# Kernel tuning notes

Hardware: AMD Instinct MI355X
Metric: run time of the kernel (lower is better)

The kernel has to match this reference:

```python
import jax, jax.numpy as jnp
import numpy as np
import math
from jax import lax

B, L, D, P, V, K = 4, 2048, 512, 128, 8, 4


def _lin(x, w, b):
    # torch Linear: y = x @ W^T + b, W shape (out, in)
    return jnp.einsum('...i,oi->...o', x, w) + b


def _gelu(v):
    return jax.nn.gelu(v, approximate=False)


def _dwconv_causal(x_ncl, w, b):
    # depthwise causal conv: torch Conv1d(groups=D, padding=K-1) then [:, :, :L]
    y = lax.conv_general_dilated(x_ncl, w, (1,), [(K - 1, 0)],
                                 dimension_numbers=('NCH', 'OIH', 'NCH'),
                                 feature_group_count=D)
    return y + b[None, :, None]


def _ln(v, g, b):
    m = v.mean(-1, keepdims=True)
    var = v.var(-1, keepdims=True)
    return (v - m) / jnp.sqrt(var + 1e-5) * g + b


def setup_inputs() -> dict:
    key = jax.random.key(0)
    it = iter(jax.random.split(key, 64))
    def nrm(shape, s=0.02):
        return jax.random.normal(next(it), shape, dtype=jnp.float32) * s
    z = lambda *s: jnp.zeros(s, jnp.float32)
    return dict(
        x=nrm((B, L, D), 1.0),
        lc_w=nrm((D, 1, K)), lc_b=z(D),
        cg_w=nrm((D, 1, K)), cg_b=z(D),
        cp_w=nrm((D, D)), cp_b=z(D),
        tw_w=nrm((D, D)), tw_b=z(D),
        omega_scale=jnp.full((D,), 0.01, jnp.float32),
        pi0_w=nrm((D, D)), pi0_b=z(D),
        pi2_w=nrm((D, D)), pi2_b=z(D),
        m1v_w=nrm((D, D)), m1v_b=z(D),
        m1o_w=nrm((D, D)), m1o_b=z(D),
        mag_w=nrm((D, D)), mag_b=z(D),
        mag_scale=jnp.asarray(5.0, jnp.float32),
        qo_w=nrm((D, D)), qo_b=z(D),
        ke_w=nrm((P, D)), ke_b=z(P),
        ve_w=nrm((V, D)), ve_b=z(V),
        sk0_w=nrm((D, 2 * D)), sk0_b=z(D),
        sk2_w=nrm((P, D)), sk2_b=z(P),
        sg_w=nrm((1, D)), sg_b=z(1),
        kvo_w=nrm((D, V)), kvo_b=z(D),
        ln_g=jnp.ones(5 * D, jnp.float32), ln_b=z(5 * D),
        o1_w=nrm((2 * D, 5 * D)), o1_b=z(2 * D),
        o2_w=nrm((D, 2 * D)), o2_b=z(D),
    )


def reference(x, lc_w, lc_b, cg_w, cg_b, cp_w, cp_b, tw_w, tw_b, omega_scale,
              pi0_w, pi0_b, pi2_w, pi2_b, m1v_w, m1v_b, m1o_w, m1o_b,
              mag_w, mag_b, mag_scale, qo_w, qo_b, ke_w, ke_b, ve_w, ve_b,
              sk0_w, sk0_b, sk2_w, sk2_b, sg_w, sg_b, kvo_w, kvo_b,
              ln_g, ln_b, o1_w, o1_b, o2_w, o2_b):
    Bs, Ls, Ds = x.shape
    # local gated causal depthwise conv branch
    xc = jnp.transpose(x, (0, 2, 1))                          # (B, D, L)
    co = _dwconv_causal(xc, lc_w, lc_b)
    cg = jax.nn.sigmoid(_dwconv_causal(xc, cg_w, cg_b))
    conv_out = _lin(jnp.transpose(co * cg, (0, 2, 1)), cp_w, cp_b)
    # evolving phases
    omega_scaled = _lin(x, tw_w, tw_b) * jnp.abs(omega_scale)
    phi = _lin(_gelu(_lin(x, pi0_w, pi0_b)), pi2_w, pi2_b) + jnp.cumsum(omega_scaled, axis=1)
    cos_phi = jnp.cos(phi)
    sin_phi = jnp.sin(phi)
    # magnitude-weighted phase memory
    v1 = _lin(x, m1v_w, m1v_b)
    magnitude = jax.nn.sigmoid(_lin(x, mag_w, mag_b)) * jnp.abs(mag_scale)
    wv1 = magnitude * v1
    sqrt_mag = jnp.sqrt(jnp.cumsum(magnitude, axis=1) + 1e-8)
    mem1_cos = jnp.cumsum(wv1 * cos_phi, axis=1) / sqrt_mag
    mem1_sin = jnp.cumsum(wv1 * sin_phi, axis=1) / sqrt_mag
    phi_q = phi + _lin(x, qo_w, qo_b)
    pos_ret = (mem1_cos * jnp.cos(phi_q) + mem1_sin * jnp.sin(phi_q)) / math.sqrt(Ds)
    pos_out = _lin(pos_ret, m1o_w, m1o_b)
    # phase-keyed associative KV memory
    query_phase = jnp.tanh(_lin(x, ke_w, ke_b)) * math.pi    # (B, L, P)
    values = _lin(x, ve_w, ve_b)                              # (B, L, V)
    store_gate = jax.nn.sigmoid(_lin(x, sg_w, sg_b))          # (B, L, 1)
    positions = jnp.arange(1, Ls + 1, dtype=x.dtype).reshape(1, -1, 1)
    context_avg = jnp.cumsum(x, axis=1) / positions
    storage_phase = jnp.tanh(_lin(_gelu(_lin(jnp.concatenate([x, context_avg], -1), sk0_w, sk0_b)), sk2_w, sk2_b)) * math.pi
    gated_vals = values * store_gate                          # (B, L, V)
    kv_mem_cos = jnp.cumsum(jnp.cos(storage_phase)[..., None] * gated_vals[:, :, None, :], axis=1)
    kv_mem_sin = jnp.cumsum(jnp.sin(storage_phase)[..., None] * gated_vals[:, :, None, :], axis=1)
    gate_norm = jnp.sqrt(jnp.maximum(jnp.cumsum(store_gate, axis=1), 1.0))[..., None]  # (B, L, 1, 1)
    kv_mem_cos = kv_mem_cos / gate_norm
    kv_mem_sin = kv_mem_sin / gate_norm
    kv_retrieved = (jnp.cos(query_phase)[..., None] * kv_mem_cos +
                    jnp.sin(query_phase)[..., None] * kv_mem_sin).sum(axis=2) / math.sqrt(P)
    kv_out = _lin(kv_retrieved, kvo_w, kvo_b)
    # combine (dropout is identity in eval)
    combined = jnp.concatenate([conv_out, pos_out, kv_out, x * cos_phi, x * sin_phi], axis=-1)
    h = _ln(combined, ln_g, ln_b)
    h = _lin(_gelu(_lin(h, o1_w, o1_b)), o2_w, o2_b)
    return x + h
```

## Files before the change

kernel.cpp:

```cpp
#include <hip/hip_runtime.h>
#include <cstdint>

typedef unsigned short u16;
typedef short short8 __attribute__((ext_vector_type(8)));
typedef float floatx4 __attribute__((ext_vector_type(4)));

#define B_ 4
#define L_ 2048
#define D_ 512
#define P_ 128
#define V_ 8
#define BL (B_ * L_)
#define NC_ 128
#define CH_ 16
#define PI_F 3.14159265358979323846f

__device__ inline u16 f2b(float f) {
    unsigned u = __float_as_uint(f);
    unsigned r = u + 0x7FFFu + ((u >> 16) & 1u);
    return (u16)(r >> 16);
}
__device__ inline float b2f(u16 h) {
    return __uint_as_float(((unsigned)h) << 16);
}
__device__ inline float gelu_f(float v) {
    return 0.5f * v * (1.0f + erff(v * 0.70710678118654752f));
}
__device__ inline float sigm(float v) {
    return 1.0f / (1.0f + __expf(-v));
}
__device__ inline float tanh_fast(float v) {
    return 1.0f - 2.0f / (1.0f + __expf(2.0f * v));
}

__device__ inline void async16(const u16* g, u16* l) {
    __builtin_amdgcn_global_load_lds(
        (const __attribute__((address_space(1))) unsigned int*)g,
        (__attribute__((address_space(3))) unsigned int*)l, 16, 0, 0);
}

extern __shared__ u16 smem_dyn[];

enum { EPI_F32 = 0, EPI_BF16 = 1, EPI_GELU_BF16 = 2, EPI_RESID_F32 = 3,
       EPI_PASS1 = 4, EPI_ATOMIC = 5 };

template <int EPI>
__device__ __forceinline__ void gemm_body(
    const u16* __restrict__ A, int lda,
    const u16* __restrict__ W, int ldw,
    const float* __restrict__ bias,
    void* __restrict__ Cout, int ldc, int N, int K,
    const float* __restrict__ resid, int mt, int nt)
{
    const int tid  = threadIdx.x;
    const int lane = tid & 63;
    const int wid  = tid >> 6;
    const int wm   = wid & 1, wn = wid >> 1;
    const int l16  = lane & 15, quad = lane >> 4;
    const int rswz = (l16 >> 1) & 3;

    floatx4 acc[4][2] = {};

    const u16* Ab = A + (size_t)(mt * 128) * lda;
    const u16* Wb = W + (size_t)(nt * 128) * ldw;

    const int srow = lane >> 2;
    const int scol = ((lane & 3) ^ ((srow >> 1) & 3)) * 8;
    const u16* ga0 = Ab + (size_t)(wid * 16 + srow) * lda + scol;
    const u16* gb0 = Wb + (size_t)(wid * 16 + srow) * ldw + scol;
    const int lW = wid * 512;

    const int nsteps = K >> 5;

    auto stage = [&](int t, int s) {
        u16* base = smem_dyn + s * 8192;
        const int ko = t * 32;
        async16(ga0 + ko, base + lW);
        async16(gb0 + ko, base + 4096 + lW);
    };

    auto readfrag = [&](int slot, short8 (&a)[4], short8 (&b)[2]) {
        const u16* As = smem_dyn + slot * 8192;
        const u16* Bs = As + 4096;
#pragma unroll
        for (int i = 0; i < 4; i++)
            a[i] = *(const short8*)(&As[(wm * 64 + i * 16 + l16) * 32 + (quad ^ rswz) * 8]);
#pragma unroll
        for (int j = 0; j < 2; j++)
            b[j] = *(const short8*)(&Bs[(wn * 32 + j * 16 + l16) * 32 + (quad ^ rswz) * 8]);
    };

    auto mfma8 = [&](short8 (&a)[4], short8 (&b)[2]) {
        __builtin_amdgcn_s_setprio(1);
#pragma unroll
        for (int i = 0; i < 4; i++)
#pragma unroll
            for (int j = 0; j < 2; j++)
                acc[i][j] = __builtin_amdgcn_mfma_f32_16x16x32_bf16(a[i], b[j], acc[i][j], 0, 0, 0);
        __builtin_amdgcn_s_setprio(0);
    };

    stage(0, 0);
    if (nsteps > 1) stage(1, 1);
    if (nsteps > 2) stage(2, 2);
    if (nsteps > 2)      asm volatile("s_waitcnt vmcnt(4)" ::: "memory");
    else if (nsteps > 1) asm volatile("s_waitcnt vmcnt(2)" ::: "memory");
    else                 asm volatile("s_waitcnt vmcnt(0)" ::: "memory");
    __builtin_amdgcn_s_barrier();
    asm volatile("" ::: "memory");

    short8 aE[4], bE[2], aO[4], bO[2];
    readfrag(0, aE, bE);

    for (int t = 0; t < nsteps; t += 2) {
        asm volatile("s_waitcnt lgkmcnt(0)" ::: "memory");
        if (t + 2 < nsteps)      asm volatile("s_waitcnt vmcnt(2)" ::: "memory");
        else if (t + 1 < nsteps) asm volatile("s_waitcnt vmcnt(0)" ::: "memory");
        __builtin_amdgcn_s_barrier();
        asm volatile("" ::: "memory");
        if (t + 3 < nsteps) stage(t + 3, t % 3);
        if (t + 1 < nsteps) readfrag((t + 1) % 3, aO, bO);
        mfma8(aE, bE);
        const int t1 = t + 1;
        asm volatile("s_waitcnt lgkmcnt(0)" ::: "memory");
        if (t1 + 2 < nsteps)      asm volatile("s_waitcnt vmcnt(2)" ::: "memory");
        else if (t1 + 1 < nsteps) asm volatile("s_waitcnt vmcnt(0)" ::: "memory");
        __builtin_amdgcn_s_barrier();
        asm volatile("" ::: "memory");
        if (t1 + 3 < nsteps) stage(t1 + 3, t1 % 3);
        if (t1 + 1 < nsteps) readfrag((t1 + 1) % 3, aE, bE);
        mfma8(aO, bO);
    }

#pragma unroll
    for (int i = 0; i < 4; i++) {
#pragma unroll
        for (int j = 0; j < 2; j++) {
#pragma unroll
            for (int r = 0; r < 4; r++) {
                int grow = mt * 128 + wm * 64 + i * 16 + quad * 4 + r;
                int gcol = nt * 128 + wn * 32 + j * 16 + l16;
                if (gcol < N) {
                    float v = acc[i][j][r] + (bias ? bias[gcol] : 0.0f);
                    size_t off = (size_t)grow * ldc + gcol;
                    if (EPI == EPI_F32)            ((float*)Cout)[off] = v;
                    else if (EPI == EPI_BF16)      ((u16*)Cout)[off] = f2b(v);
                    else if (EPI == EPI_GELU_BF16) ((u16*)Cout)[off] = f2b(gelu_f(v));
                    else if (EPI == EPI_PASS1) {
                        float vv = (gcol >= 512 && gcol < 1024) ? gelu_f(v) : v;
                        ((u16*)Cout)[off] = f2b(vv);
                    }
                    else if (EPI == EPI_RESID_F32) ((float*)Cout)[off] = v + resid[off];
                    else                           atomicAdd(&((float*)Cout)[off], v);
                }
            }
        }
    }
}

template <int EPI>
__global__ __launch_bounds__(512)
void gemm256(const u16* __restrict__ A, int lda,
             const u16* __restrict__ W, int ldw,
             const float* __restrict__ bias,
             void* __restrict__ C, int ldc, int N, int K,
             const float* __restrict__ resid)
{
    int kz = blockIdx.z;
    gemm_body<EPI>(A + (size_t)kz * K, lda, W + (size_t)kz * K, ldw,
                   kz == 0 ? bias : nullptr, C, ldc, N, K, resid,
                   blockIdx.x, blockIdx.y);
}

__global__ __launch_bounds__(512)
void mega1(const u16* __restrict__ xcat, const u16* __restrict__ convg,
           const u16* __restrict__ wcat1, const float* __restrict__ bcat1,
           const u16* __restrict__ kesgw, const float* __restrict__ kesgb,
           const u16* __restrict__ cpw, const float* __restrict__ cp_b,
           u16* __restrict__ out1, float* __restrict__ kesgo, u16* __restrict__ combined)
{
    int y = blockIdx.y, mt = blockIdx.x;
    if (y < 20)
        gemm_body<EPI_PASS1>(xcat, 1024, wcat1, 512, bcat1, out1, 2560, 2560, 512, nullptr, mt, y);
    else if (y < 22)
        gemm_body<EPI_F32>(xcat, 1024, kesgw, 512, kesgb, kesgo, 144, 144, 512, nullptr, mt, y - 20);
    else
        gemm_body<EPI_BF16>(convg, 512, cpw, 512, cp_b, combined, 2560, 512, 512, nullptr, mt, y - 22);
}

__global__ __launch_bounds__(512)
void mega2(const u16* __restrict__ posret, const u16* __restrict__ xcat,
           const u16* __restrict__ m1ow, const float* __restrict__ m1o_b,
           const u16* __restrict__ sk0w, const float* __restrict__ sk0_b,
           u16* __restrict__ combined, u16* __restrict__ sk0g)
{
    int y = blockIdx.y, mt = blockIdx.x;
    if (y < 4)
        gemm_body<EPI_BF16>(posret, 512, m1ow, 512, m1o_b, combined + 512, 2560, 512, 512, nullptr, mt, y);
    else
        gemm_body<EPI_GELU_BF16>(xcat, 1024, sk0w, 1024, sk0_b, sk0g, 512, 512, 1024, nullptr, mt, y - 4);
}

__global__ __launch_bounds__(256)
void prep_weights(const float* tw, const float* pi0, const float* m1v, const float* mag, const float* qo,
                  const float* ke, const float* ve, const float* sg,
                  const float* pi2, const float* cp, const float* sk0, const float* sk2,
                  const float* m1o, const float* o1, const float* o2,
                  const float* tw_b, const float* pi0_b, const float* m1v_b, const float* mag_b, const float* qo_b,
                  const float* ke_b, const float* ve_b, const float* sg_b,
                  u16* wcat1, float* bcat1, u16* kesgw, float* kesgb,
                  u16* pi2w, u16* cpw, u16* sk0w, u16* sk2w, u16* m1ow, u16* o1w, u16* o2w)
{
    int idx = blockIdx.x * 256 + threadIdx.x;
    const int n0 = 2560 * 512;
    const int n1 = n0 + 256 * 512;
    const int n2 = n1 + 512 * 512;
    const int n3 = n2 + 512 * 512;
    const int n4 = n3 + 512 * 1024;
    const int n5 = n4 + 128 * 512;
    const int n6 = n5 + 512 * 512;
    const int n7 = n6 + 1024 * 2560;
    const int n8 = n7 + 512 * 1024;
    const int n9 = n8 + 2560;
    const int n10 = n9 + 256;
    if (idx < n0) {
        int r = idx >> 9, k = idx & 511;
        const float* s = (r < 512) ? tw : (r < 1024) ? pi0 : (r < 1536) ? m1v : (r < 2048) ? mag : qo;
        wcat1[idx] = f2b(s[(r & 511) * 512 + k]);
    } else if (idx < n1) {
        int i = idx - n0; int r = i >> 9, k = i & 511;
        float v;
        if (r < 128)      v = ke[r * 512 + k];
        else if (r < 136) v = ve[(r - 128) * 512 + k];
        else if (r == 136) v = sg[k];
        else               v = 0.0f;
        kesgw[i] = f2b(v);
    }
    else if (idx < n2) { int i = idx - n1; pi2w[i] = f2b(pi2[i]); }
    else if (idx < n3) { int i = idx - n2; cpw[i]  = f2b(cp[i]); }
    else if (idx < n4) { int i = idx - n3; sk0w[i] = f2b(sk0[i]); }
    else if (idx < n5) { int i = idx - n4; sk2w[i] = f2b(sk2[i]); }
    else if (idx < n6) { int i = idx - n5; m1ow[i] = f2b(m1o[i]); }
    else if (idx < n7) { int i = idx - n6; o1w[i]  = f2b(o1[i]); }
    else if (idx < n8) { int i = idx - n7; o2w[i]  = f2b(o2[i]); }
    else if (idx < n9) {
        int i = idx - n8;
        const float* s = (i < 512) ? tw_b : (i < 1024) ? pi0_b : (i < 1536) ? m1v_b : (i < 2048) ? mag_b : qo_b;
        bcat1[i] = s[i & 511];
    } else if (idx < n10) {
        int i = idx - n9;
        kesgb[i] = (i < 128) ? ke_b[i] : (i < 136) ? ve_b[i - 128] : (i == 136) ? sg_b[0] : 0.0f;
    }
}

__global__ __launch_bounds__(256)
void conv_gate(const float* __restrict__ x,
               const float* __restrict__ lcw, const float* __restrict__ lcb,
               const float* __restrict__ cgw, const float* __restrict__ cgb,
               u16* __restrict__ out, u16* __restrict__ xcat)
{
    int idx = blockIdx.x * 256 + threadIdx.x;
    int d = idx & 511; int bl = idx >> 9;
    int l = bl & (L_ - 1); int b = bl >> 11;
    float a0 = 0.f, a1 = 0.f, xv3 = 0.f;
#pragma unroll
    for (int k = 0; k < 4; k++) {
        int ls = l - 3 + k;
        if (ls >= 0) {
            float xv = x[((size_t)(b * L_ + ls)) * 512 + d];
            if (k == 3) xv3 = xv;
            a0 += xv * lcw[d * 4 + k];
            a1 += xv * cgw[d * 4 + k];
        }
    }
    a0 += lcb[d];
    a1 = sigm(a1 + cgb[d]);
    out[idx] = f2b(a0 * a1);
    xcat[(size_t)bl * 1024 + d] = f2b(xv3);
}

__device__ __forceinline__ void scan_a_body(
    int blk, const u16* __restrict__ out1, const float* __restrict__ x,
    const float* __restrict__ oscale, const float* __restrict__ msc,
    float* __restrict__ cs_o, float* __restrict__ cs_x, float* __restrict__ cs_m)
{
    int nc = blk & 15, dt = (blk >> 4) & 7, b = blk >> 7;
    int t = threadIdx.x; int dl = t & 63, lg = t >> 6;
    int d = dt * 64 + dl;
    float os = fabsf(oscale[d]);
    float ms = fabsf(msc[0]);
    float so = 0.f, sx = 0.f, sm = 0.f;
    int l0 = nc * 128 + lg * 16;
    for (int i = 0; i < 16; i++) {
        size_t r = (size_t)(b * L_ + l0 + i);
        so += b2f(out1[r * 2560 + d]) * os;
        sm += sigm(b2f(out1[r * 2560 + 1536 + d])) * ms;
        sx += x[r * 512 + d];
    }
    __shared__ float sh[3][8][64];
    sh[0][lg][dl] = so; sh[1][lg][dl] = sx; sh[2][lg][dl] = sm;
    __syncthreads();
    if (t < 64) {
        float a = 0.f, xx = 0.f, m = 0.f;
        for (int g = 0; g < 8; g++) { a += sh[0][g][t]; xx += sh[1][g][t]; m += sh[2][g][t]; }
        size_t o = ((size_t)(b * 16 + nc)) * 512 + dt * 64 + t;
        cs_o[o] = a; cs_x[o] = xx; cs_m[o] = m;
    }
}

__device__ __forceinline__ void gate_body(const float* __restrict__ kesgo,
                                          float* __restrict__ gni)
{
    if (threadIdx.x >= 256) return;
    int b = threadIdx.x >> 6; int lane = threadIdx.x & 63;
    float v[32]; float s = 0.f;
#pragma unroll
    for (int i = 0; i < 32; i++) {
        int l = lane * 32 + i;
        v[i] = sigm(kesgo[((size_t)(b * L_ + l)) * 144 + 136]);
        s += v[i];
    }
    float sc = s;
#pragma unroll
    for (int ofs = 1; ofs < 64; ofs <<= 1) {
        float t = __shfl_up(sc, ofs, 64);
        if (lane >= ofs) sc += t;
    }
    float run = sc - s;
#pragma unroll
    for (int i = 0; i < 32; i++) {
        run += v[i];
        gni[b * L_ + lane * 32 + i] = rsqrtf(fmaxf(run, 1.0f));
    }
}

__global__ __launch_bounds__(512)
void stage2(const u16* __restrict__ out1, const u16* __restrict__ pi2w,
            const float* __restrict__ pi2_b, u16* __restrict__ phib,
            const float* __restrict__ x, const float* __restrict__ oscale,
            const float* __restrict__ msc,
            float* __restrict__ cs_o, float* __restrict__ cs_x, float* __restrict__ cs_m,
            const float* __restrict__ kesgo, float* __restrict__ gni)
{
    int blk = blockIdx.x;
    if (blk < 256)
        gemm_body<EPI_BF16>(out1 + 512, 2560, pi2w, 512, pi2_b, phib, 512, 512, 512,
                            nullptr, blk & 63, blk >> 6);
    else if (blk < 768)
        scan_a_body(blk - 256, out1, x, oscale, msc, cs_o, cs_x, cs_m);
    else
        gate_body(kesgo, gni);
}

__global__ __launch_bounds__(256)
void scan_c(const u16* __restrict__ out1, const u16* __restrict__ phib,
            const float* __restrict__ oscale, const float* __restrict__ msc,
            const float* __restrict__ cs_o,
            float* __restrict__ phi, float* __restrict__ cs_wc, float* __restrict__ cs_ws)
{
    int blk = blockIdx.x;
    int nc = blk & 15, dt = (blk >> 4) & 7, b = blk >> 7;
    int t = threadIdx.x; int dl = t & 63, lg = t >> 6;
    int d = dt * 64 + dl;
    float os = fabsf(oscale[d]);
    float ms = fabsf(msc[0]);
    int l0 = nc * 128 + lg * 32;
    float so = 0.f;
    for (int i = 0; i < 32; i++) {
        size_t r = (size_t)(b * L_ + l0 + i);
        so += b2f(out1[r * 2560 + d]) * os;
    }
    __shared__ float sh[4][64];
    __shared__ float shw[2][4][64];
    sh[lg][dl] = so;
    __syncthreads();
    float pre = 0.f;
    for (int p = 0; p < nc; p++) pre += cs_o[((size_t)(b * 16 + p)) * 512 + d];
    for (int g = 0; g < lg; g++) pre += sh[g][dl];
    float cum = pre, swc = 0.f, sws = 0.f;
    for (int i = 0; i < 32; i++) {
        size_t r = (size_t)(b * L_ + l0 + i);
        cum += b2f(out1[r * 2560 + d]) * os;
        float ph = b2f(phib[r * 512 + d]) + cum;
        phi[r * 512 + d] = ph;
        float mg = sigm(b2f(out1[r * 2560 + 1536 + d])) * ms;
        float wv = mg * b2f(out1[r * 2560 + 1024 + d]);
        float s = __sinf(ph), c = __cosf(ph);
        swc += wv * c; sws += wv * s;
    }
    shw[0][lg][dl] = swc; shw[1][lg][dl] = sws;
    __syncthreads();
    if (t < 64) {
        float a = 0.f, bb = 0.f;
        for (int g = 0; g < 4; g++) { a += shw[0][g][t]; bb += shw[1][g][t]; }
        size_t o = ((size_t)(b * 16 + nc)) * 512 + dt * 64 + t;
        cs_wc[o] = a; cs_ws[o] = bb;
    }
}

__global__ __launch_bounds__(256)
void scan_e(const u16* __restrict__ out1, const float* __restrict__ phi,
            const float* __restrict__ x, const float* __restrict__ msc,
            const float* __restrict__ cs_m, const float* __restrict__ cs_x,
            const float* __restrict__ cs_wc, const float* __restrict__ cs_ws,
            u16* __restrict__ posret, u16* __restrict__ xcat, u16* __restrict__ combined)
{
    int blk = blockIdx.x;
    int nc = blk & 15, dt = (blk >> 4) & 7, b = blk >> 7;
    int t = threadIdx.x; int dl = t & 63, lg = t >> 6;
    int d = dt * 64 + dl;
    float ms = fabsf(msc[0]);
    int l0 = nc * 128 + lg * 32;
    float sm = 0.f, swc = 0.f, sws = 0.f, sx = 0.f;
    for (int i = 0; i < 32; i++) {
        size_t r = (size_t)(b * L_ + l0 + i);
        float ph = phi[r * 512 + d];
        float mg = sigm(b2f(out1[r * 2560 + 1536 + d])) * ms;
        float wv = mg * b2f(out1[r * 2560 + 1024 + d]);
        float s = __sinf(ph), c = __cosf(ph);
        sm += mg; swc += wv * c; sws += wv * s; sx += x[r * 512 + d];
    }
    __shared__ float sh[4][4][64];
    sh[0][lg][dl] = sm; sh[1][lg][dl] = swc; sh[2][lg][dl] = sws; sh[3][lg][dl] = sx;
    __syncthreads();
    float cm = 0.f, cwc = 0.f, cws = 0.f, cx = 0.f;
    for (int p = 0; p < nc; p++) {
        size_t o = ((size_t)(b * 16 + p)) * 512 + d;
        cm += cs_m[o]; cwc += cs_wc[o]; cws += cs_ws[o]; cx += cs_x[o];
    }
    for (int g = 0; g < lg; g++) {
        cm += sh[0][g][dl]; cwc += sh[1][g][dl]; cws += sh[2][g][dl]; cx += sh[3][g][dl];
    }
    const float invsqD = 0.044194173824159216f;
    for (int i = 0; i < 32; i++) {
        int l = l0 + i;
        size_t r = (size_t)(b * L_ + l);
        float ph = phi[r * 512 + d];
        float mg = sigm(b2f(out1[r * 2560 + 1536 + d])) * ms;
        float wv = mg * b2f(out1[r * 2560 + 1024 + d]);
        float xv = x[r * 512 + d];
        float s = __sinf(ph), c = __cosf(ph);
        cm += mg; cwc += wv * c; cws += wv * s; cx += xv;
        float smag = sqrtf(cm + 1e-8f);
        float m1c = cwc / smag, m1s = cws / smag;
        float phq = ph + b2f(out1[r * 2560 + 2048 + d]);
        float sq = __sinf(phq), cq = __cosf(phq);
        float pr = (m1c * cq + m1s * sq) * invsqD;
        posret[r * 512 + d] = f2b(pr);
        xcat[r * 1024 + 512 + d] = f2b(cx / (float)(l + 1));
        combined[r * 2560 + 1536 + d] = f2b(xv * c);
        combined[r * 2560 + 2048 + d] = f2b(xv * s);
    }
}

__global__ __launch_bounds__(64)
void kv_chunk(const float* __restrict__ sppre, const float* __restrict__ kesgo,
              float* __restrict__ spc, float* __restrict__ sps,
              float* __restrict__ csum)
{
    int blk = blockIdx.x; int nc = blk & (NC_ - 1), b = blk >> 7;
    int t = threadIdx.x;
    float Sc[2][8] = {}, Ss[2][8] = {};
    for (int i = 0; i < CH_; i++) {
        size_t r = (size_t)(b * L_ + nc * CH_ + i);
        float sgate = sigm(kesgo[r * 144 + 136]);
        float g[8];
#pragma unroll
        for (int v = 0; v < 8; v++) g[v] = kesgo[r * 144 + 128 + v] * sgate;
#pragma unroll
        for (int j = 0; j < 2; j++) {
            int p = t + j * 64;
            float sp = tanh_fast(sppre[r * 128 + p]) * PI_F;
            float s = __sinf(sp), c = __cosf(sp);
            spc[r * 128 + p] = c; sps[r * 128 + p] = s;
#pragma unroll
            for (int v = 0; v < 8; v++) { Sc[j][v] += c * g[v]; Ss[j][v] += s * g[v]; }
        }
    }
    size_t base = (size_t)blk * 2048;
#pragma unroll
    for (int j = 0; j < 2; j++)
#pragma unroll
        for (int v = 0; v < 8; v++) {
            csum[base + (t + j * 64) * 8 + v]        = Sc[j][v];
            csum[base + 1024 + (t + j * 64) * 8 + v] = Ss[j][v];
        }
}

__global__ __launch_bounds__(256)
void kv_scan(const float* __restrict__ cin, float* __restrict__ cex)
{
    int t = blockIdx.x * 256 + threadIdx.x;
    int pv = t & 1023; int cs = (t >> 10) & 1; int b = t >> 11;
    float run = 0.f;
    for (int nc = 0; nc < NC_; nc++) {
        size_t o = ((size_t)(b * NC_ + nc)) * 2048 + cs * 1024 + pv;
        cex[o] = run; run += cin[o];
    }
}

__global__ __launch_bounds__(64)
void kv_retrieve(const float* __restrict__ spc, const float* __restrict__ sps,
                 const float* __restrict__ kesgo,
                 const float* __restrict__ gni, const float* __restrict__ cex,
                 const float* __restrict__ kvo_w, const float* __restrict__ kvo_b,
                 u16* __restrict__ combined)
{
    int blk = blockIdx.x; int nc = blk & (NC_ - 1), b = blk >> 7;
    int t = threadIdx.x;
    const int nb = t * 8;
    float wr[8][8], br[8];
#pragma unroll
    for (int n = 0; n < 8; n++) {
        *(float4*)&wr[n][0] = *(const float4*)&kvo_w[(nb + n) * 8];
        *(float4*)&wr[n][4] = *(const float4*)&kvo_w[(nb + n) * 8 + 4];
        br[n] = kvo_b[nb + n];
    }
    float Sc[2][8], Ss[2][8];
    size_t base = (size_t)blk * 2048;
#pragma unroll
    for (int j = 0; j < 2; j++)
#pragma unroll
        for (int v = 0; v < 8; v++) {
            Sc[j][v] = cex[base + (t + j * 64) * 8 + v];
            Ss[j][v] = cex[base + 1024 + (t + j * 64) * 8 + v];
        }
    for (int i = 0; i < CH_; i++) {
        size_t r = (size_t)(b * L_ + nc * CH_ + i);
        float sgate = sigm(kesgo[r * 144 + 136]);
        float g[8];
#pragma unroll
        for (int v = 0; v < 8; v++) g[v] = kesgo[r * 144 + 128 + v] * sgate;
        float part[8];
#pragma unroll
        for (int v = 0; v < 8; v++) part[v] = 0.f;
#pragma unroll
        for (int j = 0; j < 2; j++) {
            int p = t + j * 64;
            float c = spc[r * 128 + p], s = sps[r * 128 + p];
#pragma unroll
            for (int v = 0; v < 8; v++) { Sc[j][v] += c * g[v]; Ss[j][v] += s * g[v]; }
            float qp = tanh_fast(kesgo[r * 144 + p]) * PI_F;
            float sq = __sinf(qp), cq = __cosf(qp);
#pragma unroll
            for (int v = 0; v < 8; v++) part[v] += cq * Sc[j][v] + sq * Ss[j][v];
        }
#pragma unroll
        for (int ofs = 1; ofs < 64; ofs <<= 1)
#pragma unroll
            for (int v = 0; v < 8; v++) part[v] += __shfl_xor(part[v], ofs, 64);
        float scale = gni[r] * 0.08838834764831845f;
        float pv[8];
#pragma unroll
        for (int v = 0; v < 8; v++) pv[v] = part[v] * scale;
        u16 outv[8];
#pragma unroll
        for (int n = 0; n < 8; n++) {
            float a = br[n];
#pragma unroll
            for (int v = 0; v < 8; v++) a += pv[v] * wr[n][v];
            outv[n] = f2b(a);
        }
        *(uint4*)&combined[r * 2560 + 1024 + nb] = *(const uint4*)outv;
    }
}

__global__ __launch_bounds__(320)
void ln_rows(u16* __restrict__ combined, const float* __restrict__ g, const float* __restrict__ bb)
{
    size_t m = blockIdx.x; int t = threadIdx.x;
    u16 vv[8];
    *(uint4*)vv = *(const uint4*)&combined[m * 2560 + t * 8];
    float f[8]; float s = 0.f, s2 = 0.f;
#pragma unroll
    for (int k = 0; k < 8; k++) { f[k] = b2f(vv[k]); s += f[k]; s2 += f[k] * f[k]; }
#pragma unroll
    for (int ofs = 1; ofs < 64; ofs <<= 1) {
        s  += __shfl_xor(s, ofs, 64);
        s2 += __shfl_xor(s2, ofs, 64);
    }
    __shared__ float shs[5], shs2[5];
    int wv = t >> 6;
    if ((t & 63) == 0) { shs[wv] = s; shs2[wv] = s2; }
    __syncthreads();
    float S = 0.f, S2 = 0.f;
#pragma unroll
    for (int i = 0; i < 5; i++) { S += shs[i]; S2 += shs2[i]; }
    float mean = S * (1.0f / 2560.0f);
    float var  = S2 * (1.0f / 2560.0f) - mean * mean;
    float rstd = rsqrtf(var + 1e-5f);
#pragma unroll
    for (int k = 0; k < 8; k++) {
        int c = t * 8 + k;
        vv[k] = f2b((f[k] - mean) * rstd * g[c] + bb[c]);
    }
    *(uint4*)&combined[m * 2560 + t * 8] = *(const uint4*)vv;
}

extern "C" void kernel_launch(void* const* d_in, const int* in_sizes, int n_in,
                              void* d_out, int out_size, void* d_ws, size_t ws_size,
                              hipStream_t stream)
{
    const float* x     = (const float*)d_in[0];
    const float* lc_w  = (const float*)d_in[1];
    const float* lc_b  = (const float*)d_in[2];
    const float* cg_w  = (const float*)d_in[3];
    const float* cg_b  = (const float*)d_in[4];
    const float* cp_w  = (const float*)d_in[5];
    const float* cp_b  = (const float*)d_in[6];
    const float* tw_w  = (const float*)d_in[7];
    const float* tw_b  = (const float*)d_in[8];
    const float* omega_scale = (const float*)d_in[9];
    const float* pi0_w = (const float*)d_in[10];
    const float* pi0_b = (const float*)d_in[11];
    const float* pi2_w = (const float*)d_in[12];
    const float* pi2_b = (const float*)d_in[13];
    const float* m1v_w = (const float*)d_in[14];
    const float* m1v_b = (const float*)d_in[15];
    const float* m1o_w = (const float*)d_in[16];
    const float* m1o_b = (const float*)d_in[17];
    const float* mag_w = (const float*)d_in[18];
    const float* mag_b = (const float*)d_in[19];
    const float* mag_scale = (const float*)d_in[20];
    const float* qo_w  = (const float*)d_in[21];
    const float* qo_b  = (const float*)d_in[22];
    const float* ke_w  = (const float*)d_in[23];
    const float* ke_b  = (const float*)d_in[24];
    const float* ve_w  = (const float*)d_in[25];
    const float* ve_b  = (const float*)d_in[26];
    const float* sk0_w = (const float*)d_in[27];
    const float* sk0_b = (const float*)d_in[28];
    const float* sk2_w = (const float*)d_in[29];
    const float* sk2_b = (const float*)d_in[30];
    const float* sg_w  = (const float*)d_in[31];
    const float* sg_b  = (const float*)d_in[32];
    const float* kvo_w = (const float*)d_in[33];
    const float* kvo_b = (const float*)d_in[34];
    const float* ln_g  = (const float*)d_in[35];
    const float* ln_b  = (const float*)d_in[36];
    const float* o1_w  = (const float*)d_in[37];
    const float* o1_b  = (const float*)d_in[38];
    const float* o2_w  = (const float*)d_in[39];
    const float* o2_b  = (const float*)d_in[40];
    float* out = (float*)d_out;

    char* base = (char*)d_ws;
    size_t off = 0;
    auto alloc = [&](size_t bytes) -> void* {
        void* p = base + off;
        off += (bytes + 255) & ~(size_t)255;
        return p;
    };

    u16*   wcat1  = (u16*)  alloc((size_t)2560 * 512 * 2);
    float* bcat1  = (float*)alloc(2560 * 4);
    u16*   kesgw  = (u16*)  alloc((size_t)256 * 512 * 2);
    float* kesgb  = (float*)alloc(256 * 4);
    u16*   pi2w   = (u16*)  alloc((size_t)512 * 512 * 2);
    u16*   cpw    = (u16*)  alloc((size_t)512 * 512 * 2);
    u16*   sk0w   = (u16*)  alloc((size_t)512 * 1024 * 2);
    u16*   sk2w   = (u16*)  alloc((size_t)128 * 512 * 2);
    u16*   m1ow   = (u16*)  alloc((size_t)512 * 512 * 2);
    u16*   o1w    = (u16*)  alloc((size_t)1024 * 2560 * 2);
    u16*   o2w    = (u16*)  alloc((size_t)512 * 1024 * 2);
    u16*   xcat   = (u16*)  alloc((size_t)BL * 1024 * 2);
    u16*   out1   = (u16*)  alloc((size_t)BL * 2560 * 2);
    u16*   phib   = (u16*)  alloc((size_t)BL * 512 * 2);
    float* phi    = (float*)alloc((size_t)BL * 512 * 4);
    float* kesgo  = (float*)alloc((size_t)BL * 144 * 4);
    u16*   convg  = (u16*)  alloc((size_t)BL * 512 * 2);
    float* sppre  = (float*)alloc((size_t)BL * 128 * 4);
    u16*   combined = (u16*)alloc((size_t)BL * 2560 * 2);
    float* cs_o   = (float*)alloc((size_t)4 * 16 * 512 * 4);
    float* cs_x   = (float*)alloc((size_t)4 * 16 * 512 * 4);
    float* cs_m   = (float*)alloc((size_t)4 * 16 * 512 * 4);
    float* cs_wc  = (float*)alloc((size_t)4 * 16 * 512 * 4);
    float* cs_ws  = (float*)alloc((size_t)4 * 16 * 512 * 4);
    float* gni    = (float*)alloc((size_t)BL * 4);
    u16*   posret = convg;
    u16*   sk0g   = out1;
    float* spc    = phi;
    float* sps    = phi + (size_t)BL * 128;
    float* kvcs   = (float*)phib;
    float* kvex   = (float*)phib + (size_t)B_ * NC_ * 2048;
    u16*   o1g    = xcat;
    (void)ws_size; (void)in_sizes; (void)n_in; (void)out_size;

    const size_t SMEM = 49152;

    prep_weights<<<23307, 256, 0, stream>>>(
        tw_w, pi0_w, m1v_w, mag_w, qo_w, ke_w, ve_w, sg_w,
        pi2_w, cp_w, sk0_w, sk2_w, m1o_w, o1_w, o2_w,
        tw_b, pi0_b, m1v_b, mag_b, qo_b, ke_b, ve_b, sg_b,
        wcat1, bcat1, kesgw, kesgb, pi2w, cpw, sk0w, sk2w, m1ow, o1w, o2w);
    conv_gate<<<16384, 256, 0, stream>>>(x, lc_w, lc_b, cg_w, cg_b, convg, xcat);
    mega1<<<dim3(64, 26), 512, SMEM, stream>>>(xcat, convg, wcat1, bcat1,
                                               kesgw, kesgb, cpw, cp_b,
                                               out1, kesgo, combined);
    stage2<<<769, 512, SMEM, stream>>>(out1, pi2w, pi2_b, phib,
                                       x, omega_scale, mag_scale,
                                       cs_o, cs_x, cs_m, kesgo, gni);
    scan_c<<<512, 256, 0, stream>>>(out1, phib, omega_scale, mag_scale, cs_o,
                                    phi, cs_wc, cs_ws);
    scan_e<<<512, 256, 0, stream>>>(out1, phi, x, mag_scale, cs_m, cs_x, cs_wc, cs_ws,
                                    posret, xcat, combined);
    mega2<<<dim3(64, 8), 512, SMEM, stream>>>(posret, xcat, m1ow, m1o_b,
                                              sk0w, sk0_b, combined, sk0g);
    hipMemsetAsync(sppre, 0, (size_t)BL * 128 * 4, stream);
    gemm256<EPI_ATOMIC><<<dim3(64, 1, 4), 512, SMEM, stream>>>(sk0g, 512, sk2w, 512, sk2_b,
                                                               sppre, 128, 128, 128, nullptr);
    kv_chunk<<<4 * NC_, 64, 0, stream>>>(sppre, kesgo, spc, sps, kvcs);
    kv_scan<<<32, 256, 0, stream>>>(kvcs, kvex);
    kv_retrieve<<<4 * NC_, 64, 0, stream>>>(spc, sps, kesgo, gni, kvex, kvo_w, kvo_b, combined);
    ln_rows<<<8192, 320, 0, stream>>>(combined, ln_g, ln_b);
    gemm256<EPI_GELU_BF16><<<dim3(64, 8), 512, SMEM, stream>>>(combined, 2560, o1w, 2560, o1_b,
                                                               o1g, 1024, 1024, 2560, nullptr);
    gemm256<EPI_RESID_F32><<<dim3(64, 4), 512, SMEM, stream>>>(o1g, 1024, o2w, 1024, o2_b,
                                                               out, 512, 512, 1024, x);
}
```

Measured before the change: 518.0 us.

## Restructure GEMM body into split-K warp groups with 64-wide K steps

The shared GEMM body now splits its 8 waves into two K-halves, each owning a 64x64 output tile (4x4 MFMA accumulators) instead of 64x32. Each K step is 64 wide with double buffering and an 8-chunk XOR swizzle, and the two halves are summed through an LDS reduction before the epilogue. The aim is more MFMA work per LDS fragment load and fewer barriers per K element, at the cost of 64KB shared memory, more registers per thread (launch bounds now 512,4), an extra reduction pass, and the loss of the previous three-stage prefetch depth.

New measurement: 567.3 us. +9.5%, slower.

```diff
diff --git a/kernel.cpp b/kernel.cpp
--- a/kernel.cpp
+++ b/kernel.cpp
@@ -55,103 +55,120 @@
     const int tid  = threadIdx.x;
     const int lane = tid & 63;
     const int wid  = tid >> 6;
-    const int wm   = wid & 1, wn = wid >> 1;
+    const int p    = wid & 3;
+    const int kh   = wid >> 2;
+    const int wm   = p & 1, wn = p >> 1;
     const int l16  = lane & 15, quad = lane >> 4;
-    const int rswz = (l16 >> 1) & 3;
-
-    floatx4 acc[4][2] = {};
+
+    floatx4 acc[4][4] = {};
 
     const u16* Ab = A + (size_t)(mt * 128) * lda;
     const u16* Wb = W + (size_t)(nt * 128) * ldw;
 
-    const int srow = lane >> 2;
-    const int scol = ((lane & 3) ^ ((srow >> 1) & 3)) * 8;
-    const u16* ga0 = Ab + (size_t)(wid * 16 + srow) * lda + scol;
-    const u16* gb0 = Wb + (size_t)(wid * 16 + srow) * ldw + scol;
-    const int lW = wid * 512;
-
-    const int nsteps = K >> 5;
+    const int srow = lane >> 3;
+    const int scol = ((lane & 7) ^ (srow & 7)) * 8;
+    const u16* ga0 = Ab + (size_t)(wid * 16 + srow)     * lda + scol;
+    const u16* ga1 = Ab + (size_t)(wid * 16 + 8 + srow) * lda + scol;
+    const u16* gb0 = Wb + (size_t)(wid * 16 + srow)     * ldw + scol;
+    const u16* gb1 = Wb + (size_t)(wid * 16 + 8 + srow) * ldw + scol;
+    const int lOff = wid * 1024;
+
+    const int ns = K >> 6;
 
     auto stage = [&](int t, int s) {
-        u16* base = smem_dyn + s * 8192;
-        const int ko = t * 32;
-        async16(ga0 + ko, base + lW);
-        async16(gb0 + ko, base + 4096 + lW);
+        u16* baseS = smem_dyn + s * 16384;
+        const int ko = t * 64;
+        async16(ga0 + ko, baseS + lOff);
+        async16(ga1 + ko, baseS + lOff + 512);
+        async16(gb0 + ko, baseS + 8192 + lOff);
+        async16(gb1 + ko, baseS + 8192 + lOff + 512);
     };
 
-    auto readfrag = [&](int slot, short8 (&a)[4], short8 (&b)[2]) {
-        const u16* As = smem_dyn + slot * 8192;
-        const u16* Bs = As + 4096;
+    const int rchunk = ((kh * 4 + quad) ^ (l16 & 7)) * 8;
+
+    short8 a[4], b[4];
+    auto readfrag = [&](int s) {
+        const u16* As = smem_dyn + s * 16384;
+        const u16* Bs = As + 8192;
 #pragma unroll
         for (int i = 0; i < 4; i++)
-            a[i] = *(const short8*)(&As[(wm * 64 + i * 16 + l16) * 32 + (quad ^ rswz) * 8]);
-#pragma unroll
-        for (int j = 0; j < 2; j++)
-            b[j] = *(const short8*)(&Bs[(wn * 32 + j * 16 + l16) * 32 + (quad ^ rswz) * 8]);
+            a[i] = *(const short8*)(&As[(wm * 64 + i * 16 + l16) * 64 + rchunk]);
+#pragma unroll
+        for (int j = 0; j < 4; j++)
+            b[j] = *(const short8*)(&Bs[(wn * 64 + j * 16 + l16) * 64 + rchunk]);
     };
 
-    auto mfma8 = [&](short8 (&a)[4], short8 (&b)[2]) {
+    auto mfma16 = [&]() {
         __builtin_amdgcn_s_setprio(1);
 #pragma unroll
         for (int i = 0; i < 4; i++)
 #pragma unroll
-            for (int j = 0; j < 2; j++)
+            for (int j = 0; j < 4; j++)
                 acc[i][j] = __builtin_amdgcn_mfma_f32_16x16x32_bf16(a[i], b[j], acc[i][j], 0, 0, 0);
         __builtin_amdgcn_s_setprio(0);
     };
 
     stage(0, 0);
-    if (nsteps > 1) stage(1, 1);
-    if (nsteps > 2) stage(2, 2);
-    if (nsteps > 2)      asm volatile("s_waitcnt vmcnt(4)" ::: "memory");
-    else if (nsteps > 1) asm volatile("s_waitcnt vmcnt(2)" ::: "memory");
-    else                 asm volatile("s_waitcnt vmcnt(0)" ::: "memory");
+    if (ns > 1) stage(1, 1);
+    if (ns > 1) asm volatile("s_waitcnt vmcnt(4)" ::: "memory");
+    else        asm volatile("s_waitcnt vmcnt(0)" ::: "memory");
     __builtin_amdgcn_s_barrier();
-    asm volatile("" ::: "memory");
-
-    short8 aE[4], bE[2], aO[4], bO[2];
-    readfrag(0, aE, bE);
-
-    for (int t = 0; t < nsteps; t += 2) {
+
+    for (int t = 0; t < ns; ++t) {
+        readfrag(t & 1);
         asm volatile("s_waitcnt lgkmcnt(0)" ::: "memory");
-        if (t + 2 < nsteps)      asm volatile("s_waitcnt vmcnt(2)" ::: "memory");
-        else if (t + 1 < nsteps) asm volatile("s_waitcnt vmcnt(0)" ::: "memory");
+        __builtin_amdgcn_sched_barrier(0);
         __builtin_amdgcn_s_barrier();
-        asm volatile("" ::: "memory");
-        if (t + 3 < nsteps) stage(t + 3, t % 3);
-        if (t + 1 < nsteps) readfrag((t + 1) % 3, aO, bO);
-        mfma8(aE, bE);
-        const int t1 = t + 1;
-        asm volatile("s_waitcnt lgkmcnt(0)" ::: "memory");
-        if (t1 + 2 < nsteps)      asm volatile("s_waitcnt vmcnt(2)" ::: "memory");
-        else if (t1 + 1 < nsteps) asm volatile("s_waitcnt vmcnt(0)" ::: "memory");
-        __builtin_amdgcn_s_barrier();
-        asm volatile("" ::: "memory");
-        if (t1 + 3 < nsteps) stage(t1 + 3, t1 % 3);
-        if (t1 + 1 < nsteps) readfrag((t1 + 1) % 3, aE, bE);
-        mfma8(aO, bO);
-    }
-
-#pragma unroll
-    for (int i = 0; i < 4; i++) {
-#pragma unroll
-        for (int j = 0; j < 2; j++) {
-#pragma unroll
-            for (int r = 0; r < 4; r++) {
-                int grow = mt * 128 + wm * 64 + i * 16 + quad * 4 + r;
-                int gcol = nt * 128 + wn * 32 + j * 16 + l16;
-                if (gcol < N) {
-                    float v = acc[i][j][r] + (bias ? bias[gcol] : 0.0f);
-                    size_t off = (size_t)grow * ldc + gcol;
-                    if (EPI == EPI_F32)            ((float*)Cout)[off] = v;
-                    else if (EPI == EPI_BF16)      ((u16*)Cout)[off] = f2b(v);
-                    else if (EPI == EPI_GELU_BF16) ((u16*)Cout)[off] = f2b(gelu_f(v));
-                    else if (EPI == EPI_PASS1) {
-                        float vv = (gcol >= 512 && gcol < 1024) ? gelu_f(v) : v;
-                        ((u16*)Cout)[off] = f2b(vv);
+        if (t + 2 < ns) stage(t + 2, t & 1);
+        mfma16();
+        if (t + 1 < ns) {
+            if (t + 2 < ns) asm volatile("s_waitcnt vmcnt(4)" ::: "memory");
+            else            asm volatile("s_waitcnt vmcnt(0)" ::: "memory");
+            __builtin_amdgcn_s_barrier();
+        }
+    }
+
+    float* red = (float*)smem_dyn;
+    if (kh == 0) {
+        float* r0 = red + wid * 4096;
+#pragma unroll
+        for (int i = 0; i < 4; i++)
+#pragma unroll
+            for (int j = 0; j < 4; j++)
+                *(floatx4*)&r0[(i * 4 + j) * 256 + lane * 4] = acc[i][j];
+    }
+    asm volatile("s_waitcnt lgkmcnt(0)" ::: "memory");
+    __builtin_amdgcn_s_barrier();
+    if (kh == 1) {
+        const float* r0 = red + p * 4096;
+#pragma unroll
+        for (int i = 0; i < 4; i++)
+#pragma unroll
+            for (int j = 0; j < 4; j++) {
+                floatx4 o = *(const floatx4*)&r0[(i * 4 + j) * 256 + lane * 4];
+                acc[i][j] += o;
+            }
+#pragma unroll
+        for (int i = 0; i < 4; i++) {
+#pragma unroll
+            for (int j = 0; j < 4; j++) {
+#pragma unroll
+                for (int r = 0; r < 4; r++) {
+                    int grow = mt * 128 + wm * 64 + i * 16 + quad * 4 + r;
+                    int gcol = nt * 128 + wn * 64 + j * 16 + l16;
+                    if (gcol < N) {
+                        float v = acc[i][j][r] + (bias ? bias[gcol] : 0.0f);
+                        size_t off = (size_t)grow * ldc + gcol;
+                        if (EPI == EPI_F32)            ((float*)Cout)[off] = v;
+                        else if (EPI == EPI_BF16)      ((u16*)Cout)[off] = f2b(v);
+                        else if (EPI == EPI_GELU_BF16) ((u16*)Cout)[off] = f2b(gelu_f(v));
+                        else if (EPI == EPI_PASS1) {
+                            float vv = (gcol >= 512 && gcol < 1024) ? gelu_f(v) : v;
+                            ((u16*)Cout)[off] = f2b(vv);
+                        }
+                        else if (EPI == EPI_RESID_F32) ((float*)Cout)[off] = v + resid[off];
+                        else                           atomicAdd(&((float*)Cout)[off], v);
                     }
-                    else if (EPI == EPI_RESID_F32) ((float*)Cout)[off] = v + resid[off];
-                    else                           atomicAdd(&((float*)Cout)[off], v);
                 }
             }
         }
@@ -159,7 +176,7 @@
 }
 
 template <int EPI>
-__global__ __launch_bounds__(512)
+__global__ __launch_bounds__(512, 4)
 void gemm256(const u16* __restrict__ A, int lda,
              const u16* __restrict__ W, int ldw,
              const float* __restrict__ bias,
@@ -172,7 +189,7 @@
                    blockIdx.x, blockIdx.y);
 }
 
-__global__ __launch_bounds__(512)
+__global__ __launch_bounds__(512, 4)
 void mega1(const u16* __restrict__ xcat, const u16* __restrict__ convg,
            const u16* __restrict__ wcat1, const float* __restrict__ bcat1,
            const u16* __restrict__ kesgw, const float* __restrict__ kesgb,
@@ -188,7 +205,7 @@
         gemm_body<EPI_BF16>(convg, 512, cpw, 512, cp_b, combined, 2560, 512, 512, nullptr, mt, y - 22);
 }
 
-__global__ __launch_bounds__(512)
+__global__ __launch_bounds__(512, 4)
 void mega2(const u16* __restrict__ posret, const u16* __restrict__ xcat,
            const u16* __restrict__ m1ow, const float* __restrict__ m1o_b,
            const u16* __restrict__ sk0w, const float* __restrict__ sk0_b,
@@ -334,7 +351,7 @@
     }
 }
 
-__global__ __launch_bounds__(512)
+__global__ __launch_bounds__(512, 4)
 void stage2(const u16* __restrict__ out1, const u16* __restrict__ pi2w,
             const float* __restrict__ pi2_b, u16* __restrict__ phib,
             const float* __restrict__ x, const float* __restrict__ oscale,
@@ -686,7 +703,7 @@
     u16*   o1g    = xcat;
     (void)ws_size; (void)in_sizes; (void)n_in; (void)out_size;
 
-    const size_t SMEM = 49152;
+    const size_t SMEM = 65536;
 
     prep_weights<<<23307, 256, 0, stream>>>(
         tw_w, pi0_w, m1v_w, mag_w, qo_w, ke_w, ve_w, sg_w,
```
